# Kernel tuning notes

Measured on AMD Instinct MI355X. Metric: run time of the kernel, lower is better.

The kernel has to match this reference:

```python
import jax, jax.numpy as jnp
import numpy as np

B, E, CIN, C, PRE, DME, DEN = 8, 64, 128, 128, 128, 32, 32
N_EDGE_TYPES, N_PATH_TYPES = 10, 20


def leaky(v):
    return jnp.where(v >= 0, v, 0.1 * v)


def setup_inputs() -> dict:
    key = jax.random.key(0)
    ks = jax.random.split(key, 30)
    s = 0.05
    inp = {
        'x': jax.random.normal(ks[0], (B, CIN, E), jnp.float32),
        'y': jax.random.normal(ks[1], (B, CIN, E), jnp.float32),
        'm_bias_mat': jax.random.normal(ks[2], (B, E, E), jnp.float32),
        'edge_mat': jax.random.randint(ks[3], (B, E, E), 0, N_EDGE_TYPES),
        'p_bias_mat': jax.random.normal(ks[4], (B, E, E, E), jnp.float32),
        'path_mat': jax.random.randint(ks[5], (B, E, E, E), 0, N_PATH_TYPES),
        'pre_out': jax.random.normal(ks[6], (B, PRE, E, E), jnp.float32),
        # parameters (conv1d/conv2d k=1 weights squeezed to matrices/vectors)
        'xc1_w': jax.random.normal(ks[7], (C, CIN), jnp.float32) * s,
        'yc1_w': jax.random.normal(ks[8], (C, CIN), jnp.float32) * s,
        'xc2_w': jax.random.normal(ks[9], (C,), jnp.float32) * s,
        'xc2_b': jax.random.normal(ks[10], (1,), jnp.float32) * s,
        'yc2_w': jax.random.normal(ks[11], (C,), jnp.float32) * s,
        'yc2_b': jax.random.normal(ks[12], (1,), jnp.float32) * s,
        'pconv_w': jax.random.normal(ks[13], (DEN,), jnp.float32) * s,
        'econv_w': jax.random.normal(ks[14], (DME,), jnp.float32) * s,
        'conv1_w': jax.random.normal(ks[15], (C, 2 * C + PRE), jnp.float32) * s,
        'conv1_b': jax.random.normal(ks[16], (C,), jnp.float32) * s,
        'conv2_w': jax.random.normal(ks[17], (C, C, 3, 3), jnp.float32) * s,
        'conv2_b': jax.random.normal(ks[18], (C,), jnp.float32) * s,
        'score_w': jax.random.normal(ks[19], (C,), jnp.float32) * s,
        'xlin_w': jax.random.normal(ks[20], (CIN, CIN), jnp.float32) * s,
        'ylin_w': jax.random.normal(ks[21], (CIN, CIN), jnp.float32) * s,
        'edge_table': jax.random.normal(ks[22], (N_EDGE_TYPES, DME), jnp.float32) * s,
        'path_table': jax.random.normal(ks[23], (N_PATH_TYPES, DEN), jnp.float32) * s,
    }
    return inp


def reference(x, y, m_bias_mat, edge_mat, p_bias_mat, path_mat, pre_out,
              xc1_w, yc1_w, xc2_w, xc2_b, yc2_w, yc2_b, pconv_w, econv_w,
              conv1_w, conv1_b, conv2_w, conv2_b, score_w, xlin_w, ylin_w,
              edge_table, path_table):
    # x,y: [B, CIN, E]; M == N == entity_num == E (required by path_fea reshape)
    x_f = jnp.einsum('ci,bim->bcm', xc1_w, x)                    # [B,C,M]
    y_f = jnp.einsum('ci,bin->bcn', yc1_w, y)                    # [B,C,N]
    x_self = jnp.einsum('c,bcm->bm', xc2_w, x_f) + xc2_b         # [B,M]
    y_other = jnp.einsum('c,bcn->bn', yc2_w, y_f) + yc2_b        # [B,N]
    # torch broadcast: [B,1,M] + [B,N,1] -> [B,N,M]
    logist = leaky(x_self[:, None, :] + y_other[:, :, None])     # [B,E,E]

    # ---- per-entity path attention (vectorized over entity axis e) ----
    path_embed = path_table[path_mat]                            # [B,E,M,N,DEN]
    path_logist = leaky(jnp.einsum('bemnd,d->bemn', path_embed, pconv_w))
    local = logist[:, None, :, :] + path_logist + p_bias_mat     # [B,E,M,N]
    A = jax.nn.softmax(local, axis=-1)
    x_ret = leaky(jnp.einsum('bemn,bcn->bcem', A, y_f) + x_f[:, :, None, :])  # [B,C,E,M]
    A2 = jax.nn.softmax(jnp.swapaxes(local, 2, 3), axis=-1)
    y_ret = leaky(jnp.einsum('benm,bcm->bcen', A2, x_f) + y_f[:, :, None, :])  # [B,C,E,N]
    path_fea = jnp.concatenate([x_ret, y_ret], axis=1)           # [B,2C,E,E]

    men = jnp.concatenate([path_fea, pre_out], axis=1)           # [B,2C+PRE,E,E]
    h = leaky(jnp.einsum('oc,bcij->boij', conv1_w, men) + conv1_b[None, :, None, None])
    h = jax.lax.conv_general_dilated(h, conv2_w, (1, 1), 'SAME',
                                     dimension_numbers=('NCHW', 'OIHW', 'NCHW'))
    men2rel = leaky(h + conv2_b[None, :, None, None])            # [B,C,E,E]

    scores = leaky(jnp.einsum('c,bcij->bij', score_w, men2rel))  # [B,E,E]
    edge_logist = leaky(jnp.einsum('bmnd,d->bmn', edge_table[edge_mat], econv_w))
    g = logist + scores + edge_logist + m_bias_mat               # [B,E,E]

    x_lin = jnp.einsum('ij,bjm->bmi', xlin_w, x)                 # [B,M,CIN]
    y_lin = jnp.einsum('ij,bjn->bni', ylin_w, y)                 # [B,N,CIN]
    G = jax.nn.softmax(g, axis=-1)
    out_x = jnp.einsum('bmn,bni->bim', G, y_lin) + x             # residual, [B,CIN,M]
    G2 = jax.nn.softmax(jnp.swapaxes(g, 1, 2), axis=-1)
    out_y = jnp.einsum('bnm,bmi->bin', G2, x_lin) + y            # [B,CIN,N]
    return (out_x, out_y, men2rel)
```

## Files before the change

### kernel.cpp

```cpp
#include <hip/hip_runtime.h>
#include <hip/hip_bf16.h>


typedef unsigned short u16;
typedef unsigned int u32;
typedef short s16x8 __attribute__((ext_vector_type(8)));
typedef float f32x4 __attribute__((ext_vector_type(4)));

__device__ __forceinline__ float b2f(u16 u) { return __uint_as_float(((u32)u) << 16); }
__device__ __forceinline__ u16 f2b(float f) {
    u32 x = __float_as_uint(f);
    u32 r = (x + 0x7fffu + ((x >> 16) & 1u)) >> 16;
    return (u16)r;
}
__device__ __forceinline__ float lk(float v) { return v >= 0.f ? v : 0.1f * v; }
__device__ __forceinline__ s16x8 cvt8(const float* p) {
    float4 a = ((const float4*)p)[0], c = ((const float4*)p)[1];
    s16x8 r;
    r[0] = (short)f2b(a.x); r[1] = (short)f2b(a.y); r[2] = (short)f2b(a.z); r[3] = (short)f2b(a.w);
    r[4] = (short)f2b(c.x); r[5] = (short)f2b(c.y); r[6] = (short)f2b(c.z); r[7] = (short)f2b(c.w);
    return r;
}

__global__ __launch_bounds__(256) void k_prep(const float* __restrict__ w1, const float* __restrict__ w2,
                                              u16* __restrict__ wA1, u16* __restrict__ wA2,
                                              const float* __restrict__ x, const float* __restrict__ y,
                                              const float* __restrict__ xc1, const float* __restrict__ yc1,
                                              const float* __restrict__ xc2w, const float* __restrict__ xc2b,
                                              const float* __restrict__ yc2w, const float* __restrict__ yc2b,
                                              const float* __restrict__ xlw, const float* __restrict__ ylw,
                                              u16* __restrict__ xfb, u16* __restrict__ yfb,
                                              float* __restrict__ xfT, float* __restrict__ yfT,
                                              u16* __restrict__ xlT, u16* __restrict__ ylT,
                                              float* __restrict__ Xs, float* __restrict__ Yo,
                                              const float* __restrict__ pre, u16* __restrict__ menT) {
    int bid = blockIdx.x;
    int t = threadIdx.x;
    if (bid < 768) {
        int idx = bid * 256 + t;
        if (idx < 49152) {
            int e = idx & 7, lane = (idx >> 3) & 63, mtg = (idx >> 9) & 7, kc = idx >> 12;
            int o = mtg * 16 + (lane & 15), c = kc * 32 + ((lane >> 4) << 3) + e;
            wA1[idx] = f2b(w1[o * 384 + c]);
        } else {
            int id2 = idx - 49152;
            if (id2 < 147456) {
                int e = id2 & 7, lane = (id2 >> 3) & 63, mtg = (id2 >> 9) & 7;
                int kc = (id2 >> 12) & 3, tap = id2 >> 14;
                int o = mtg * 16 + (lane & 15), c = kc * 32 + ((lane >> 4) << 3) + e;
                wA2[id2] = f2b(w2[(o * 128 + c) * 9 + tap]);
            }
        }
        return;
    }
    if (bid < 800) {
        int r = bid - 768;
        int b = r >> 2, g4 = r & 3;
        int lane = t & 63, w = t >> 6, l15 = lane & 15, q4 = lane >> 4;
        __shared__ u16 sT[64][136];
        const float* src = (g4 == 0 || g4 == 2) ? x : y;
        const float* wptr = (g4 == 0) ? xc1 : (g4 == 1) ? yc1 : (g4 == 2) ? xlw : ylw;
        {
            int i = t >> 1, m0 = (t & 1) * 32;
            const float4* ps = (const float4*)(src + (b * 128 + i) * 64 + m0);
#pragma unroll
            for (int q = 0; q < 8; ++q) {
                float4 v = ps[q];
                int m = m0 + q * 4;
                sT[m + 0][i] = f2b(v.x); sT[m + 1][i] = f2b(v.y);
                sT[m + 2][i] = f2b(v.z); sT[m + 3][i] = f2b(v.w);
            }
        }
        __syncthreads();
        int m = w * 16 + l15;
        f32x4 acc[8];
#pragma unroll
        for (int mt = 0; mt < 8; ++mt) acc[mt] = (f32x4)(0.f);
#pragma unroll
        for (int kt = 0; kt < 4; ++kt) {
            s16x8 bfr = *(const s16x8*)&sT[m][kt * 32 + q4 * 8];
#pragma unroll
            for (int mt = 0; mt < 8; ++mt) {
                s16x8 af = cvt8(wptr + (mt * 16 + l15) * 128 + kt * 32 + q4 * 8);
                acc[mt] = __builtin_amdgcn_mfma_f32_16x16x32_bf16(af, bfr, acc[mt], 0, 0, 0);
            }
        }
        if (g4 == 0 || g4 == 1) {
            u16* fb = (g4 == 0) ? xfb : yfb;
            float* fT = (g4 == 0) ? xfT : yfT;
            const float* c2w = (g4 == 0) ? xc2w : yc2w;
            const float* c2b = (g4 == 0) ? xc2b : yc2b;
            float* dvec = (g4 == 0) ? Xs : Yo;
            float sp = 0.f;
#pragma unroll
            for (int mt = 0; mt < 8; ++mt) {
                int c0 = mt * 16 + q4 * 4;
                f32x4 a = acc[mt];
                fb[(b * 128 + c0 + 0) * 64 + m] = f2b(a[0]);
                fb[(b * 128 + c0 + 1) * 64 + m] = f2b(a[1]);
                fb[(b * 128 + c0 + 2) * 64 + m] = f2b(a[2]);
                fb[(b * 128 + c0 + 3) * 64 + m] = f2b(a[3]);
                *(float4*)(fT + (b * 64 + m) * 128 + c0) = make_float4(a[0], a[1], a[2], a[3]);
                float4 wv = *(const float4*)(c2w + c0);
                sp += wv.x * a[0] + wv.y * a[1] + wv.z * a[2] + wv.w * a[3];
            }
            sp += __shfl_xor(sp, 16);
            sp += __shfl_xor(sp, 32);
            if (q4 == 0) dvec[b * 64 + m] = sp + c2b[0];
        } else {
            u16* lT = (g4 == 2) ? xlT : ylT;
#pragma unroll
            for (int mt = 0; mt < 8; ++mt) {
                int i0 = mt * 16 + q4 * 4;
                f32x4 a = acc[mt];
                lT[(b * 128 + i0 + 0) * 64 + m] = f2b(a[0]);
                lT[(b * 128 + i0 + 1) * 64 + m] = f2b(a[1]);
                lT[(b * 128 + i0 + 2) * 64 + m] = f2b(a[2]);
                lT[(b * 128 + i0 + 3) * 64 + m] = f2b(a[3]);
            }
        }
        return;
    }
    {
        int r = bid - 800;
        int b = r >> 6, i = r & 63;
        int j = t & 63, pg = t >> 6;
#pragma unroll
        for (int oc = 0; oc < 4; ++oc) {
            int p0 = pg * 32 + oc * 8;
            s16x8 v;
#pragma unroll
            for (int k = 0; k < 8; ++k)
                v[k] = (short)f2b(pre[((b * 128 + p0 + k) * 64 + i) * 64 + j]);
            *(s16x8*)(menT + ((b * 64 + i) * 64 + j) * 384 + 256 + p0) = v;
        }
    }
}

__global__ __launch_bounds__(256) void k_attn(const float* __restrict__ Xs, const float* __restrict__ Yo,
                                              const u16* __restrict__ xfb, const u16* __restrict__ yfb,
                                              const float* __restrict__ xfT, const float* __restrict__ yfT,
                                              const int* __restrict__ path_mat, const float* __restrict__ p_bias,
                                              const float* __restrict__ ptab, const float* __restrict__ pconv,
                                              u16* __restrict__ menT) {
    int b = blockIdx.x >> 6, e = blockIdx.x & 63;
    int t = threadIdx.x;
    int lane = t & 63, w = t >> 6;
    __shared__ float sA[64][68];
    __shared__ u16 Abf[64][72];
    __shared__ u16 E2bf[64][72];
    __shared__ float sRed[256];
    __shared__ float sPdot[20];
    __shared__ float sXv[64], sYv[64];

    if (t < 20) {
        float s = 0.f;
        for (int d = 0; d < 32; ++d) s += ptab[t * 32 + d] * pconv[d];
        sPdot[t] = lk(s);
    } else if (t >= 64 && t < 128) {
        sXv[t - 64] = Xs[b * 64 + t - 64];
    } else if (t >= 128 && t < 192) {
        sYv[t - 128] = Yo[b * 64 + t - 128];
    }
    __syncthreads();

    {
        int m = t >> 2, n0 = (t & 3) * 16;
        int base = (((b * 64 + e) * 64 + m) * 64 + n0);
        const int4* pm4 = (const int4*)(path_mat + base);
        const float4* pb4 = (const float4*)(p_bias + base);
        float yom = sYv[m];
#pragma unroll
        for (int q = 0; q < 4; ++q) {
            int4 pm = pm4[q]; float4 pb = pb4[q];
            int n = n0 + q * 4;
            float4 v;
            v.x = lk(sXv[n + 0] + yom) + sPdot[pm.x] + pb.x;
            v.y = lk(sXv[n + 1] + yom) + sPdot[pm.y] + pb.y;
            v.z = lk(sXv[n + 2] + yom) + sPdot[pm.z] + pb.z;
            v.w = lk(sXv[n + 3] + yom) + sPdot[pm.w] + pb.w;
            *(float4*)&sA[m][n] = v;
        }
    }
    __syncthreads();

    if (t < 128) {
        int r = t >> 1, h = t & 1;
        const float4* rp = (const float4*)&sA[r][h * 32];
        float mx = -1e30f;
#pragma unroll
        for (int k = 0; k < 8; ++k) {
            float4 v = rp[k];
            mx = fmaxf(mx, fmaxf(fmaxf(v.x, v.y), fmaxf(v.z, v.w)));
        }
        mx = fmaxf(mx, __shfl_xor(mx, 1));
        float s = 0.f;
#pragma unroll
        for (int k = 0; k < 8; ++k) {
            float4 v = rp[k];
            s += __expf(v.x - mx) + __expf(v.y - mx) + __expf(v.z - mx) + __expf(v.w - mx);
        }
        s += __shfl_xor(s, 1);
        if (h == 0) { sRed[r] = mx; sRed[64 + r] = 1.f / s; }
    } else {
        int n = (t - 128) >> 1, h = t & 1;
        float mx = -1e30f;
#pragma unroll
        for (int k = 0; k < 32; ++k) mx = fmaxf(mx, sA[h * 32 + k][n]);
        mx = fmaxf(mx, __shfl_xor(mx, 1));
        float s = 0.f;
#pragma unroll
        for (int k = 0; k < 32; ++k) s += __expf(sA[h * 32 + k][n] - mx);
        s += __shfl_xor(s, 1);
        if (h == 0) { sRed[128 + n] = mx; sRed[192 + n] = 1.f / s; }
    }
    __syncthreads();

    {
        int m = t >> 2, q = t & 3;
        float rmax = sRed[m], rinv = sRed[64 + m];
        const float4* rp = (const float4*)&sA[m][q * 16];
#pragma unroll
        for (int g2 = 0; g2 < 2; ++g2) {
            float4 v0 = rp[g2 * 2], v1 = rp[g2 * 2 + 1];
            s16x8 pk;
            pk[0] = (short)f2b(__expf(v0.x - rmax) * rinv);
            pk[1] = (short)f2b(__expf(v0.y - rmax) * rinv);
            pk[2] = (short)f2b(__expf(v0.z - rmax) * rinv);
            pk[3] = (short)f2b(__expf(v0.w - rmax) * rinv);
            pk[4] = (short)f2b(__expf(v1.x - rmax) * rinv);
            pk[5] = (short)f2b(__expf(v1.y - rmax) * rinv);
            pk[6] = (short)f2b(__expf(v1.z - rmax) * rinv);
            pk[7] = (short)f2b(__expf(v1.w - rmax) * rinv);
            *(s16x8*)&Abf[m][q * 16 + g2 * 8] = pk;
        }
    }
    {
        int n = t >> 2, q = t & 3;
        float cmax = sRed[128 + n], cinv = sRed[192 + n];
#pragma unroll
        for (int g2 = 0; g2 < 2; ++g2) {
            s16x8 pk;
#pragma unroll
            for (int k = 0; k < 8; ++k) {
                float v = sA[q * 16 + g2 * 8 + k][n];
                pk[k] = (short)f2b(__expf(v - cmax) * cinv);
            }
            *(s16x8*)&E2bf[n][q * 16 + g2 * 8] = pk;
        }
    }
    __syncthreads();

    int l15 = lane & 15, q4 = lane >> 4;
    {
        f32x4 acc[2][4];
#pragma unroll
        for (int ci = 0; ci < 2; ++ci)
#pragma unroll
            for (int mt = 0; mt < 4; ++mt) acc[ci][mt] = (f32x4)(0.f);
#pragma unroll
        for (int kt = 0; kt < 2; ++kt) {
            s16x8 afr[2];
#pragma unroll
            for (int ci = 0; ci < 2; ++ci) {
                int c = (2 * w + ci) * 16 + l15;
                afr[ci] = *(const s16x8*)(yfb + (b * 128 + c) * 64 + kt * 32 + q4 * 8);
            }
            s16x8 bfr[4];
#pragma unroll
            for (int mt = 0; mt < 4; ++mt)
                bfr[mt] = *(const s16x8*)&Abf[mt * 16 + l15][kt * 32 + q4 * 8];
#pragma unroll
            for (int ci = 0; ci < 2; ++ci)
#pragma unroll
                for (int mt = 0; mt < 4; ++mt)
                    acc[ci][mt] = __builtin_amdgcn_mfma_f32_16x16x32_bf16(afr[ci], bfr[mt], acc[ci][mt], 0, 0, 0);
        }
#pragma unroll
        for (int ci = 0; ci < 2; ++ci) {
            int c0 = (2 * w + ci) * 16 + q4 * 4;
#pragma unroll
            for (int mt = 0; mt < 4; ++mt) {
                int m = mt * 16 + l15;
                float4 res = *(const float4*)(xfT + (b * 64 + m) * 128 + c0);
                f32x4 a = acc[ci][mt];
                u32 lo = (u32)f2b(lk(a[0] + res.x)) | ((u32)f2b(lk(a[1] + res.y)) << 16);
                u32 hi = (u32)f2b(lk(a[2] + res.z)) | ((u32)f2b(lk(a[3] + res.w)) << 16);
                *(uint2*)(menT + ((b * 64 + e) * 64 + m) * 384 + c0) = make_uint2(lo, hi);
            }
        }
    }
    {
        f32x4 acc[2][4];
#pragma unroll
        for (int ci = 0; ci < 2; ++ci)
#pragma unroll
            for (int nt = 0; nt < 4; ++nt) acc[ci][nt] = (f32x4)(0.f);
#pragma unroll
        for (int kt = 0; kt < 2; ++kt) {
            s16x8 afr[2];
#pragma unroll
            for (int ci = 0; ci < 2; ++ci) {
                int c = (2 * w + ci) * 16 + l15;
                afr[ci] = *(const s16x8*)(xfb + (b * 128 + c) * 64 + kt * 32 + q4 * 8);
            }
            s16x8 bfr[4];
#pragma unroll
            for (int nt = 0; nt < 4; ++nt)
                bfr[nt] = *(const s16x8*)&E2bf[nt * 16 + l15][kt * 32 + q4 * 8];
#pragma unroll
            for (int ci = 0; ci < 2; ++ci)
#pragma unroll
                for (int nt = 0; nt < 4; ++nt)
                    acc[ci][nt] = __builtin_amdgcn_mfma_f32_16x16x32_bf16(afr[ci], bfr[nt], acc[ci][nt], 0, 0, 0);
        }
#pragma unroll
        for (int ci = 0; ci < 2; ++ci) {
            int c0 = (2 * w + ci) * 16 + q4 * 4;
#pragma unroll
            for (int nt = 0; nt < 4; ++nt) {
                int n = nt * 16 + l15;
                float4 res = *(const float4*)(yfT + (b * 64 + n) * 128 + c0);
                f32x4 a = acc[ci][nt];
                u32 lo = (u32)f2b(lk(a[0] + res.x)) | ((u32)f2b(lk(a[1] + res.y)) << 16);
                u32 hi = (u32)f2b(lk(a[2] + res.z)) | ((u32)f2b(lk(a[3] + res.w)) << 16);
                *(uint2*)(menT + ((b * 64 + e) * 64 + n) * 384 + 128 + c0) = make_uint2(lo, hi);
            }
        }
    }
}

__global__ __launch_bounds__(256) void k_conv1(const u16* __restrict__ menT, const u16* __restrict__ wA1,
                                               const float* __restrict__ b1, u16* __restrict__ hT) {
    int b = blockIdx.x >> 6, i = blockIdx.x & 63;
    int t = threadIdx.x;
    int lane = t & 63, w = t >> 6, wm = w & 1, wn = w >> 1;
    int l15 = lane & 15, q4 = lane >> 4;

    f32x4 acc[4][2];
#pragma unroll
    for (int mt = 0; mt < 4; ++mt)
#pragma unroll
        for (int nt = 0; nt < 2; ++nt) acc[mt][nt] = (f32x4)(0.f);

    const u16* mrow = menT + (b * 64 + i) * 64 * 384;
    for (int kc = 0; kc < 12; ++kc) {
        s16x8 af[4];
#pragma unroll
        for (int mt = 0; mt < 4; ++mt)
            af[mt] = *(const s16x8*)(wA1 + (((kc * 8 + wm * 4 + mt) * 64 + lane) << 3));
        s16x8 bf[2];
#pragma unroll
        for (int nt = 0; nt < 2; ++nt) {
            int j = (wn * 2 + nt) * 16 + l15;
            bf[nt] = *(const s16x8*)(mrow + j * 384 + kc * 32 + q4 * 8);
        }
#pragma unroll
        for (int mt = 0; mt < 4; ++mt)
#pragma unroll
            for (int nt = 0; nt < 2; ++nt)
                acc[mt][nt] = __builtin_amdgcn_mfma_f32_16x16x32_bf16(af[mt], bf[nt], acc[mt][nt], 0, 0, 0);
    }

#pragma unroll
    for (int mt = 0; mt < 4; ++mt) {
        int o0 = (wm * 4 + mt) * 16 + q4 * 4;
        float4 bb = *(const float4*)(b1 + o0);
#pragma unroll
        for (int nt = 0; nt < 2; ++nt) {
            int j = (wn * 2 + nt) * 16 + l15;
            f32x4 a = acc[mt][nt];
            u32 lo = (u32)f2b(lk(a[0] + bb.x)) | ((u32)f2b(lk(a[1] + bb.y)) << 16);
            u32 hi = (u32)f2b(lk(a[2] + bb.z)) | ((u32)f2b(lk(a[3] + bb.w)) << 16);
            *(uint2*)(hT + ((b * 64 + i) * 64 + j) * 128 + o0) = make_uint2(lo, hi);
        }
    }
}

__global__ __launch_bounds__(256) void k_conv2(const u16* __restrict__ hT, const u16* __restrict__ wA2,
                                               const float* __restrict__ b2, const float* __restrict__ score_w,
                                               const float* __restrict__ Xs, const float* __restrict__ Yo,
                                               const float* __restrict__ etab, const float* __restrict__ econv,
                                               const int* __restrict__ edge_mat, const float* __restrict__ m_bias,
                                               float* __restrict__ m2r, float* __restrict__ g) {
    int b = blockIdx.x >> 6, i = blockIdx.x & 63;
    int t = threadIdx.x;
    int lane = t & 63, w = t >> 6, wm = w & 1, wn = w >> 1;
    int l15 = lane & 15, q4 = lane >> 4;
    __shared__ u16 sB2[3][66][136];
    __shared__ float sSc[2][64];
    __shared__ float sEd[16];

    if (t >= 240 && t < 250) {
        int et = t - 240;
        float s = 0.f;
        for (int d = 0; d < 32; ++d) s += etab[et * 32 + d] * econv[d];
        sEd[et] = lk(s);
    }
#pragma unroll
    for (int q = 0; q < 2; ++q) {
        int u = q * 256 + t;
        if (u < 384) {
            int r = u >> 7, rem = u & 127, hcol = rem >> 6, c2 = rem & 63;
            *(u32*)&sB2[r][hcol ? 65 : 0][c2 * 2] = 0u;
        }
    }
#pragma unroll
    for (int it = 0; it < 12; ++it) {
        int u = it * 256 + t;
        int cg = u & 15, j = (u >> 4) & 63, r = u >> 10;
        int ir = i - 1 + r;
        int4 v = make_int4(0, 0, 0, 0);
        if (ir >= 0 && ir < 64)
            v = *(const int4*)(hT + ((b * 64 + ir) * 64 + j) * 128 + cg * 8);
        *(int4*)&sB2[r][j + 1][cg * 8] = v;
    }
    __syncthreads();

    f32x4 acc[4][2];
#pragma unroll
    for (int mt = 0; mt < 4; ++mt)
#pragma unroll
        for (int nt = 0; nt < 2; ++nt) acc[mt][nt] = (f32x4)(0.f);

    for (int kc = 0; kc < 4; ++kc) {
#pragma unroll
        for (int tap = 0; tap < 9; ++tap) {
            int di = tap / 3, dj = tap % 3;
            s16x8 af[4];
#pragma unroll
            for (int mt = 0; mt < 4; ++mt)
                af[mt] = *(const s16x8*)(wA2 + ((((tap * 4 + kc) * 8 + wm * 4 + mt) * 64 + lane) << 3));
#pragma unroll
            for (int nt = 0; nt < 2; ++nt) {
                int jin = wn * 32 + nt * 16 + l15 + dj;
                s16x8 bf = *(const s16x8*)(&sB2[di][jin][kc * 32 + q4 * 8]);
#pragma unroll
                for (int mt = 0; mt < 4; ++mt)
                    acc[mt][nt] = __builtin_amdgcn_mfma_f32_16x16x32_bf16(af[mt], bf, acc[mt][nt], 0, 0, 0);
            }
        }
    }

    float part[2] = {0.f, 0.f};
#pragma unroll
    for (int mt = 0; mt < 4; ++mt) {
        int o0 = wm * 64 + mt * 16 + q4 * 4;
        float4 bb = *(const float4*)(b2 + o0);
        float4 sw = *(const float4*)(score_w + o0);
#pragma unroll
        for (int nt = 0; nt < 2; ++nt) {
            int j = wn * 32 + nt * 16 + l15;
            f32x4 a = acc[mt][nt];
            float v0 = lk(a[0] + bb.x), v1 = lk(a[1] + bb.y);
            float v2 = lk(a[2] + bb.z), v3 = lk(a[3] + bb.w);
            float* dst = m2r + ((b * 128 + o0) * 64 + i) * 64 + j;
            dst[0] = v0; dst[4096] = v1; dst[8192] = v2; dst[12288] = v3;
            part[nt] += sw.x * v0 + sw.y * v1 + sw.z * v2 + sw.w * v3;
        }
    }
#pragma unroll
    for (int nt = 0; nt < 2; ++nt) {
        float p = part[nt];
        p += __shfl_xor(p, 16);
        p += __shfl_xor(p, 32);
        if (q4 == 0) sSc[wm][wn * 32 + nt * 16 + l15] = p;
    }
    __syncthreads();
    if (t < 64) {
        float s = sSc[0][t] + sSc[1][t];
        int gi = (b * 64 + i) * 64 + t;
        float L = lk(Xs[b * 64 + t] + Yo[b * 64 + i]);
        g[gi] = L + sEd[edge_mat[gi]] + m_bias[gi] + lk(s);
    }
}

__global__ __launch_bounds__(256) void k_gout(const float* __restrict__ g,
                                              const u16* __restrict__ xlT, const u16* __restrict__ ylT,
                                              const float* __restrict__ x, const float* __restrict__ y,
                                              float* __restrict__ out) {
    int b = blockIdx.x >> 1, which = blockIdx.x & 1;
    int t = threadIdx.x;
    int lane = t & 63, w = t >> 6, l15 = lane & 15, q4 = lane >> 4;
    __shared__ float sG[64][68];
    __shared__ u16 Gbf[64][72];
    __shared__ float sRed[128];

#pragma unroll
    for (int r = 0; r < 16; ++r) {
        int idx = r * 256 + t;
        sG[idx >> 6][idx & 63] = g[b * 4096 + idx];
    }
    __syncthreads();

    if (which == 0) {
        if (t < 128) {
            int r = t >> 1, h = t & 1;
            const float4* rp = (const float4*)&sG[r][h * 32];
            float mx = -1e30f;
#pragma unroll
            for (int k = 0; k < 8; ++k) {
                float4 v = rp[k];
                mx = fmaxf(mx, fmaxf(fmaxf(v.x, v.y), fmaxf(v.z, v.w)));
            }
            mx = fmaxf(mx, __shfl_xor(mx, 1));
            float s = 0.f;
#pragma unroll
            for (int k = 0; k < 8; ++k) {
                float4 v = rp[k];
                s += __expf(v.x - mx) + __expf(v.y - mx) + __expf(v.z - mx) + __expf(v.w - mx);
            }
            s += __shfl_xor(s, 1);
            if (h == 0) { sRed[r] = mx; sRed[64 + r] = 1.f / s; }
        }
        __syncthreads();
        int m = t >> 2, q = t & 3;
        float rmax = sRed[m], rinv = sRed[64 + m];
        const float4* rp = (const float4*)&sG[m][q * 16];
#pragma unroll
        for (int g2 = 0; g2 < 2; ++g2) {
            float4 v0 = rp[g2 * 2], v1 = rp[g2 * 2 + 1];
            s16x8 pk;
            pk[0] = (short)f2b(__expf(v0.x - rmax) * rinv);
            pk[1] = (short)f2b(__expf(v0.y - rmax) * rinv);
            pk[2] = (short)f2b(__expf(v0.z - rmax) * rinv);
            pk[3] = (short)f2b(__expf(v0.w - rmax) * rinv);
            pk[4] = (short)f2b(__expf(v1.x - rmax) * rinv);
            pk[5] = (short)f2b(__expf(v1.y - rmax) * rinv);
            pk[6] = (short)f2b(__expf(v1.z - rmax) * rinv);
            pk[7] = (short)f2b(__expf(v1.w - rmax) * rinv);
            *(s16x8*)&Gbf[m][q * 16 + g2 * 8] = pk;
        }
    } else {
        if (t < 128) {
            int n = t >> 1, h = t & 1;
            float mx = -1e30f;
#pragma unroll
            for (int k = 0; k < 32; ++k) mx = fmaxf(mx, sG[h * 32 + k][n]);
            mx = fmaxf(mx, __shfl_xor(mx, 1));
            float s = 0.f;
#pragma unroll
            for (int k = 0; k < 32; ++k) s += __expf(sG[h * 32 + k][n] - mx);
            s += __shfl_xor(s, 1);
            if (h == 0) { sRed[n] = mx; sRed[64 + n] = 1.f / s; }
        }
        __syncthreads();
        int n = t >> 2, q = t & 3;
        float cmax = sRed[n], cinv = sRed[64 + n];
#pragma unroll
        for (int g2 = 0; g2 < 2; ++g2) {
            s16x8 pk;
#pragma unroll
            for (int k = 0; k < 8; ++k) {
                float v = sG[q * 16 + g2 * 8 + k][n];
                pk[k] = (short)f2b(__expf(v - cmax) * cinv);
            }
            *(s16x8*)&Gbf[n][q * 16 + g2 * 8] = pk;
        }
    }
    __syncthreads();

    const u16* lT = which ? xlT : ylT;
    const float* res = which ? y : x;
    int off = which ? 65536 : 0;
    int mcol = w * 16 + l15;
    f32x4 acc[8];
#pragma unroll
    for (int mt = 0; mt < 8; ++mt) acc[mt] = (f32x4)(0.f);
#pragma unroll
    for (int kt = 0; kt < 2; ++kt) {
        s16x8 bfr = *(const s16x8*)&Gbf[mcol][kt * 32 + q4 * 8];
#pragma unroll
        for (int mt = 0; mt < 8; ++mt) {
            s16x8 af = *(const s16x8*)(lT + (b * 128 + mt * 16 + l15) * 64 + kt * 32 + q4 * 8);
            acc[mt] = __builtin_amdgcn_mfma_f32_16x16x32_bf16(af, bfr, acc[mt], 0, 0, 0);
        }
    }
#pragma unroll
    for (int mt = 0; mt < 8; ++mt) {
        int i0 = mt * 16 + q4 * 4;
        f32x4 a = acc[mt];
#pragma unroll
        for (int r = 0; r < 4; ++r) {
            int ad = (b * 128 + i0 + r) * 64 + mcol;
            out[off + ad] = a[r] + res[ad];
        }
    }
}

extern "C" void kernel_launch(void* const* d_in, const int* in_sizes, int n_in,
                              void* d_out, int out_size, void* d_ws, size_t ws_size,
                              hipStream_t stream) {
    const float* x = (const float*)d_in[0];
    const float* y = (const float*)d_in[1];
    const float* m_bias = (const float*)d_in[2];
    const int* edge_mat = (const int*)d_in[3];
    const float* p_bias = (const float*)d_in[4];
    const int* path_mat = (const int*)d_in[5];
    const float* pre = (const float*)d_in[6];
    const float* xc1 = (const float*)d_in[7];
    const float* yc1 = (const float*)d_in[8];
    const float* xc2w = (const float*)d_in[9];
    const float* xc2b = (const float*)d_in[10];
    const float* yc2w = (const float*)d_in[11];
    const float* yc2b = (const float*)d_in[12];
    const float* pconv = (const float*)d_in[13];
    const float* econv = (const float*)d_in[14];
    const float* w1 = (const float*)d_in[15];
    const float* b1 = (const float*)d_in[16];
    const float* w2 = (const float*)d_in[17];
    const float* b2 = (const float*)d_in[18];
    const float* score_w = (const float*)d_in[19];
    const float* xlw = (const float*)d_in[20];
    const float* ylw = (const float*)d_in[21];
    const float* etab = (const float*)d_in[22];
    const float* ptab = (const float*)d_in[23];

    float* Xs = (float*)d_ws;
    float* Yo = Xs + 512;
    float* g = Yo + 512;
    float* xfT = g + 32768;
    float* yfT = xfT + 65536;
    u16* wA1 = (u16*)(yfT + 65536);
    u16* wA2 = wA1 + 49152;
    u16* xfb = wA2 + 147456;
    u16* yfb = xfb + 65536;
    u16* xlT = yfb + 65536;
    u16* ylT = xlT + 65536;
    u16* menT = ylT + 65536;
    u16* hT = menT + 12582912;

    float* out = (float*)d_out;
    float* out_m2r = out + 131072;

    hipLaunchKernelGGL(k_prep, dim3(1312), dim3(256), 0, stream, w1, w2, wA1, wA2,
                       x, y, xc1, yc1, xc2w, xc2b, yc2w, yc2b, xlw, ylw,
                       xfb, yfb, xfT, yfT, xlT, ylT, Xs, Yo, pre, menT);
    hipLaunchKernelGGL(k_attn, dim3(512), dim3(256), 0, stream, Xs, Yo, xfb, yfb, xfT, yfT,
                       path_mat, p_bias, ptab, pconv, menT);
    hipLaunchKernelGGL(k_conv1, dim3(512), dim3(256), 0, stream, menT, wA1, b1, hT);
    hipLaunchKernelGGL(k_conv2, dim3(512), dim3(256), 0, stream, hT, wA2, b2, score_w,
                       Xs, Yo, etab, econv, edge_mat, m_bias, out_m2r, g);
    hipLaunchKernelGGL(k_gout, dim3(16), dim3(256), 0, stream, g, xlT, ylT, x, y, out);
}
```

Measured before the change: 190.5 us.

## Fuse conv1 into attention kernel and use zero-padded hidden buffer for conv2

The 1x1 conv1 now runs inside the attention kernel, which reads the path features for one row from shared memory instead of writing and re-reading a large global menT buffer. Only the pre_out slice is kept in global memory as a transposed bf16 buffer. The hidden activations are written into a buffer with a zero border, whose edges the prep kernel clears. This lets conv2 read its B fragments straight from global memory without LDS staging or bounds checks. The trade-offs are that conv2 now relies on cache for the 3x3 tap reuse, and the attention kernel carries more registers and shared memory.

```diff
diff --git a/kernel.cpp b/kernel.cpp
--- a/kernel.cpp
+++ b/kernel.cpp
@@ -33,7 +33,8 @@
                                               float* __restrict__ xfT, float* __restrict__ yfT,
                                               u16* __restrict__ xlT, u16* __restrict__ ylT,
                                               float* __restrict__ Xs, float* __restrict__ Yo,
-                                              const float* __restrict__ pre, u16* __restrict__ menT) {
+                                              const float* __restrict__ pre, u16* __restrict__ preT,
+                                              u16* __restrict__ hTp) {
     int bid = blockIdx.x;
     int t = threadIdx.x;
     if (bid < 768) {
@@ -121,7 +122,7 @@
         }
         return;
     }
-    {
+    if (bid < 1312) {
         int r = bid - 800;
         int b = r >> 6, i = r & 63;
         int j = t & 63, pg = t >> 6;
@@ -132,21 +133,42 @@
 #pragma unroll
             for (int k = 0; k < 8; ++k)
                 v[k] = (short)f2b(pre[((b * 128 + p0 + k) * 64 + i) * 64 + j]);
-            *(s16x8*)(menT + ((b * 64 + i) * 64 + j) * 384 + 256 + p0) = v;
-        }
+            *(s16x8*)(preT + ((b * 64 + i) * 64 + j) * 128 + p0) = v;
+        }
+        return;
+    }
+    {
+        int gid = (bid - 1312) * 256 + t;
+        int b = gid / 16640;
+        int r = gid - b * 16640;
+        u32 idx;
+        if (r < 8448) {
+            int row = r / 4224, rem = r - row * 4224;
+            int jj = rem >> 6, o2 = rem & 63;
+            idx = (u32)(((b * 66 + (row ? 65 : 0)) * 66 + jj) * 64 + o2);
+        } else {
+            int r2 = r - 8448;
+            int ii = r2 >> 7, rem = r2 & 127;
+            int side = rem >> 6, o2 = rem & 63;
+            idx = (u32)(((b * 66 + ii + 1) * 66 + (side ? 65 : 0)) * 64 + o2);
+        }
+        ((u32*)hTp)[idx] = 0u;
     }
 }
 
-__global__ __launch_bounds__(256) void k_attn(const float* __restrict__ Xs, const float* __restrict__ Yo,
-                                              const u16* __restrict__ xfb, const u16* __restrict__ yfb,
-                                              const float* __restrict__ xfT, const float* __restrict__ yfT,
-                                              const int* __restrict__ path_mat, const float* __restrict__ p_bias,
-                                              const float* __restrict__ ptab, const float* __restrict__ pconv,
-                                              u16* __restrict__ menT) {
+__global__ __launch_bounds__(256) void k_attnc(const float* __restrict__ Xs, const float* __restrict__ Yo,
+                                               const u16* __restrict__ xfb, const u16* __restrict__ yfb,
+                                               const float* __restrict__ xfT, const float* __restrict__ yfT,
+                                               const int* __restrict__ path_mat, const float* __restrict__ p_bias,
+                                               const float* __restrict__ ptab, const float* __restrict__ pconv,
+                                               const u16* __restrict__ preT, const u16* __restrict__ wA1,
+                                               const float* __restrict__ b1, u16* __restrict__ hTp) {
     int b = blockIdx.x >> 6, e = blockIdx.x & 63;
     int t = threadIdx.x;
     int lane = t & 63, w = t >> 6;
-    __shared__ float sA[64][68];
+    __shared__ __align__(16) char smem0[64 * 264 * 2];
+    float* sAf = (float*)smem0;
+    u16* sMen = (u16*)smem0;
     __shared__ u16 Abf[64][72];
     __shared__ u16 E2bf[64][72];
     __shared__ float sRed[256];
@@ -179,14 +201,14 @@
             v.y = lk(sXv[n + 1] + yom) + sPdot[pm.y] + pb.y;
             v.z = lk(sXv[n + 2] + yom) + sPdot[pm.z] + pb.z;
             v.w = lk(sXv[n + 3] + yom) + sPdot[pm.w] + pb.w;
-            *(float4*)&sA[m][n] = v;
+            *(float4*)&sAf[m * 68 + n] = v;
         }
     }
     __syncthreads();
 
     if (t < 128) {
         int r = t >> 1, h = t & 1;
-        const float4* rp = (const float4*)&sA[r][h * 32];
+        const float4* rp = (const float4*)&sAf[r * 68 + h * 32];
         float mx = -1e30f;
 #pragma unroll
         for (int k = 0; k < 8; ++k) {
@@ -206,11 +228,11 @@
         int n = (t - 128) >> 1, h = t & 1;
         float mx = -1e30f;
 #pragma unroll
-        for (int k = 0; k < 32; ++k) mx = fmaxf(mx, sA[h * 32 + k][n]);
+        for (int k = 0; k < 32; ++k) mx = fmaxf(mx, sAf[(h * 32 + k) * 68 + n]);
         mx = fmaxf(mx, __shfl_xor(mx, 1));
         float s = 0.f;
 #pragma unroll
-        for (int k = 0; k < 32; ++k) s += __expf(sA[h * 32 + k][n] - mx);
+        for (int k = 0; k < 32; ++k) s += __expf(sAf[(h * 32 + k) * 68 + n] - mx);
         s += __shfl_xor(s, 1);
         if (h == 0) { sRed[128 + n] = mx; sRed[192 + n] = 1.f / s; }
     }
@@ -219,7 +241,7 @@
     {
         int m = t >> 2, q = t & 3;
         float rmax = sRed[m], rinv = sRed[64 + m];
-        const float4* rp = (const float4*)&sA[m][q * 16];
+        const float4* rp = (const float4*)&sAf[m * 68 + q * 16];
 #pragma unroll
         for (int g2 = 0; g2 < 2; ++g2) {
             float4 v0 = rp[g2 * 2], v1 = rp[g2 * 2 + 1];
@@ -243,7 +265,7 @@
             s16x8 pk;
 #pragma unroll
             for (int k = 0; k < 8; ++k) {
-                float v = sA[q * 16 + g2 * 8 + k][n];
+                float v = sAf[(q * 16 + g2 * 8 + k) * 68 + n];
                 pk[k] = (short)f2b(__expf(v - cmax) * cinv);
             }
             *(s16x8*)&E2bf[n][q * 16 + g2 * 8] = pk;
@@ -286,7 +308,7 @@
                 f32x4 a = acc[ci][mt];
                 u32 lo = (u32)f2b(lk(a[0] + res.x)) | ((u32)f2b(lk(a[1] + res.y)) << 16);
                 u32 hi = (u32)f2b(lk(a[2] + res.z)) | ((u32)f2b(lk(a[3] + res.w)) << 16);
-                *(uint2*)(menT + ((b * 64 + e) * 64 + m) * 384 + c0) = make_uint2(lo, hi);
+                *(uint2*)&sMen[m * 264 + c0] = make_uint2(lo, hi);
             }
         }
     }
@@ -324,60 +346,55 @@
                 f32x4 a = acc[ci][nt];
                 u32 lo = (u32)f2b(lk(a[0] + res.x)) | ((u32)f2b(lk(a[1] + res.y)) << 16);
                 u32 hi = (u32)f2b(lk(a[2] + res.z)) | ((u32)f2b(lk(a[3] + res.w)) << 16);
-                *(uint2*)(menT + ((b * 64 + e) * 64 + n) * 384 + 128 + c0) = make_uint2(lo, hi);
+                *(uint2*)&sMen[n * 264 + 128 + c0] = make_uint2(lo, hi);
+            }
+        }
+    }
+    __syncthreads();
+
+    {
+        int wm = w & 1, wn = w >> 1;
+        f32x4 acc[4][2];
+#pragma unroll
+        for (int mt = 0; mt < 4; ++mt)
+#pragma unroll
+            for (int nt = 0; nt < 2; ++nt) acc[mt][nt] = (f32x4)(0.f);
+        const u16* prow = preT + (b * 64 + e) * 64 * 128;
+        for (int kc = 0; kc < 12; ++kc) {
+            s16x8 af[4];
+#pragma unroll
+            for (int mt = 0; mt < 4; ++mt)
+                af[mt] = *(const s16x8*)(wA1 + (((kc * 8 + wm * 4 + mt) * 64 + lane) << 3));
+            s16x8 bf[2];
+#pragma unroll
+            for (int nt = 0; nt < 2; ++nt) {
+                int j = (wn * 2 + nt) * 16 + l15;
+                bf[nt] = (kc < 8) ? *(const s16x8*)&sMen[j * 264 + kc * 32 + q4 * 8]
+                                  : *(const s16x8*)(prow + j * 128 + (kc - 8) * 32 + q4 * 8);
+            }
+#pragma unroll
+            for (int mt = 0; mt < 4; ++mt)
+#pragma unroll
+                for (int nt = 0; nt < 2; ++nt)
+                    acc[mt][nt] = __builtin_amdgcn_mfma_f32_16x16x32_bf16(af[mt], bf[nt], acc[mt][nt], 0, 0, 0);
+        }
+#pragma unroll
+        for (int mt = 0; mt < 4; ++mt) {
+            int o0 = (wm * 4 + mt) * 16 + q4 * 4;
+            float4 bb = *(const float4*)(b1 + o0);
+#pragma unroll
+            for (int nt = 0; nt < 2; ++nt) {
+                int j = (wn * 2 + nt) * 16 + l15;
+                f32x4 a = acc[mt][nt];
+                u32 lo = (u32)f2b(lk(a[0] + bb.x)) | ((u32)f2b(lk(a[1] + bb.y)) << 16);
+                u32 hi = (u32)f2b(lk(a[2] + bb.z)) | ((u32)f2b(lk(a[3] + bb.w)) << 16);
+                *(uint2*)(hTp + ((b * 66 + e + 1) * 66 + j + 1) * 128 + o0) = make_uint2(lo, hi);
             }
         }
     }
 }
 
-__global__ __launch_bounds__(256) void k_conv1(const u16* __restrict__ menT, const u16* __restrict__ wA1,
-                                               const float* __restrict__ b1, u16* __restrict__ hT) {
-    int b = blockIdx.x >> 6, i = blockIdx.x & 63;
-    int t = threadIdx.x;
-    int lane = t & 63, w = t >> 6, wm = w & 1, wn = w >> 1;
-    int l15 = lane & 15, q4 = lane >> 4;
-
-    f32x4 acc[4][2];
-#pragma unroll
-    for (int mt = 0; mt < 4; ++mt)
-#pragma unroll
-        for (int nt = 0; nt < 2; ++nt) acc[mt][nt] = (f32x4)(0.f);
-
-    const u16* mrow = menT + (b * 64 + i) * 64 * 384;
-    for (int kc = 0; kc < 12; ++kc) {
-        s16x8 af[4];
-#pragma unroll
-        for (int mt = 0; mt < 4; ++mt)
-            af[mt] = *(const s16x8*)(wA1 + (((kc * 8 + wm * 4 + mt) * 64 + lane) << 3));
-        s16x8 bf[2];
-#pragma unroll
-        for (int nt = 0; nt < 2; ++nt) {
-            int j = (wn * 2 + nt) * 16 + l15;
-            bf[nt] = *(const s16x8*)(mrow + j * 384 + kc * 32 + q4 * 8);
-        }
-#pragma unroll
-        for (int mt = 0; mt < 4; ++mt)
-#pragma unroll
-            for (int nt = 0; nt < 2; ++nt)
-                acc[mt][nt] = __builtin_amdgcn_mfma_f32_16x16x32_bf16(af[mt], bf[nt], acc[mt][nt], 0, 0, 0);
-    }
-
-#pragma unroll
-    for (int mt = 0; mt < 4; ++mt) {
-        int o0 = (wm * 4 + mt) * 16 + q4 * 4;
-        float4 bb = *(const float4*)(b1 + o0);
-#pragma unroll
-        for (int nt = 0; nt < 2; ++nt) {
-            int j = (wn * 2 + nt) * 16 + l15;
-            f32x4 a = acc[mt][nt];
-            u32 lo = (u32)f2b(lk(a[0] + bb.x)) | ((u32)f2b(lk(a[1] + bb.y)) << 16);
-            u32 hi = (u32)f2b(lk(a[2] + bb.z)) | ((u32)f2b(lk(a[3] + bb.w)) << 16);
-            *(uint2*)(hT + ((b * 64 + i) * 64 + j) * 128 + o0) = make_uint2(lo, hi);
-        }
-    }
-}
-
-__global__ __launch_bounds__(256) void k_conv2(const u16* __restrict__ hT, const u16* __restrict__ wA2,
+__global__ __launch_bounds__(256) void k_conv2(const u16* __restrict__ hTp, const u16* __restrict__ wA2,
                                                const float* __restrict__ b2, const float* __restrict__ score_w,
                                                const float* __restrict__ Xs, const float* __restrict__ Yo,
                                                const float* __restrict__ etab, const float* __restrict__ econv,
@@ -387,7 +404,6 @@
     int t = threadIdx.x;
     int lane = t & 63, w = t >> 6, wm = w & 1, wn = w >> 1;
     int l15 = lane & 15, q4 = lane >> 4;
-    __shared__ u16 sB2[3][66][136];
     __shared__ float sSc[2][64];
     __shared__ float sEd[16];
 
@@ -397,25 +413,6 @@
         for (int d = 0; d < 32; ++d) s += etab[et * 32 + d] * econv[d];
         sEd[et] = lk(s);
     }
-#pragma unroll
-    for (int q = 0; q < 2; ++q) {
-        int u = q * 256 + t;
-        if (u < 384) {
-            int r = u >> 7, rem = u & 127, hcol = rem >> 6, c2 = rem & 63;
-            *(u32*)&sB2[r][hcol ? 65 : 0][c2 * 2] = 0u;
-        }
-    }
-#pragma unroll
-    for (int it = 0; it < 12; ++it) {
-        int u = it * 256 + t;
-        int cg = u & 15, j = (u >> 4) & 63, r = u >> 10;
-        int ir = i - 1 + r;
-        int4 v = make_int4(0, 0, 0, 0);
-        if (ir >= 0 && ir < 64)
-            v = *(const int4*)(hT + ((b * 64 + ir) * 64 + j) * 128 + cg * 8);
-        *(int4*)&sB2[r][j + 1][cg * 8] = v;
-    }
-    __syncthreads();
 
     f32x4 acc[4][2];
 #pragma unroll
@@ -433,8 +430,8 @@
                 af[mt] = *(const s16x8*)(wA2 + ((((tap * 4 + kc) * 8 + wm * 4 + mt) * 64 + lane) << 3));
 #pragma unroll
             for (int nt = 0; nt < 2; ++nt) {
-                int jin = wn * 32 + nt * 16 + l15 + dj;
-                s16x8 bf = *(const s16x8*)(&sB2[di][jin][kc * 32 + q4 * 8]);
+                int j = wn * 32 + nt * 16 + l15;
+                s16x8 bf = *(const s16x8*)(hTp + ((b * 66 + i + di) * 66 + j + dj) * 128 + kc * 32 + q4 * 8);
 #pragma unroll
                 for (int mt = 0; mt < 4; ++mt)
                     acc[mt][nt] = __builtin_amdgcn_mfma_f32_16x16x32_bf16(af[mt], bf, acc[mt][nt], 0, 0, 0);
@@ -627,19 +624,18 @@
     u16* yfb = xfb + 65536;
     u16* xlT = yfb + 65536;
     u16* ylT = xlT + 65536;
-    u16* menT = ylT + 65536;
-    u16* hT = menT + 12582912;
+    u16* preT = ylT + 65536;
+    u16* hTp = preT + 4194304;
 
     float* out = (float*)d_out;
     float* out_m2r = out + 131072;
 
-    hipLaunchKernelGGL(k_prep, dim3(1312), dim3(256), 0, stream, w1, w2, wA1, wA2,
+    hipLaunchKernelGGL(k_prep, dim3(1832), dim3(256), 0, stream, w1, w2, wA1, wA2,
                        x, y, xc1, yc1, xc2w, xc2b, yc2w, yc2b, xlw, ylw,
-                       xfb, yfb, xfT, yfT, xlT, ylT, Xs, Yo, pre, menT);
-    hipLaunchKernelGGL(k_attn, dim3(512), dim3(256), 0, stream, Xs, Yo, xfb, yfb, xfT, yfT,
-                       path_mat, p_bias, ptab, pconv, menT);
-    hipLaunchKernelGGL(k_conv1, dim3(512), dim3(256), 0, stream, menT, wA1, b1, hT);
-    hipLaunchKernelGGL(k_conv2, dim3(512), dim3(256), 0, stream, hT, wA2, b2, score_w,
+                       xfb, yfb, xfT, yfT, xlT, ylT, Xs, Yo, pre, preT, hTp);
+    hipLaunchKernelGGL(k_attnc, dim3(512), dim3(256), 0, stream, Xs, Yo, xfb, yfb, xfT, yfT,
+                       path_mat, p_bias, ptab, pconv, preT, wA1, b1, hTp);
+    hipLaunchKernelGGL(k_conv2, dim3(512), dim3(256), 0, stream, hTp, wA2, b2, score_w,
                        Xs, Yo, etab, econv, edge_mat, m_bias, out_m2r, g);
     hipLaunchKernelGGL(k_gout, dim3(16), dim3(256), 0, stream, g, xlT, ylT, x, y, out);
 }
```

New measurement: 190.4 us. Within noise of the previous version (-0.0%).
